# Kernel optimization log

Hardware: AMD Instinct MI355X
Metric: run time of the kernel (lower is better)

## Reference

```python
import jax, jax.numpy as jnp
import numpy as np

N_NODES = 50000
N_EDGES = 800000
F_IN, F_MID, F_OUT = 256, 128, 40


def gcn_conv(x, W, b, src, dst, n_nodes):
    # GCNConv (PyG defaults): add self-loops, symmetric normalization,
    # linear transform, scatter-sum to targets, then bias.
    h = x @ W  # [N, F_out]
    loop = jnp.arange(n_nodes, dtype=src.dtype)
    s = jnp.concatenate([src, loop])  # sources incl. self-loops
    d = jnp.concatenate([dst, loop])  # targets incl. self-loops
    deg = jax.ops.segment_sum(jnp.ones_like(d, dtype=h.dtype), d, num_segments=n_nodes)
    dinv = jnp.where(deg > 0, jax.lax.rsqrt(deg), 0.0)
    norm = dinv[s] * dinv[d]  # [E+N]
    msgs = h[s] * norm[:, None]  # [E+N, F_out]
    out = jax.ops.segment_sum(msgs, d, num_segments=n_nodes)
    return out + b


def setup_inputs() -> dict:
    key = jax.random.key(0)
    ks = jax.random.split(key, 8)
    x = jax.random.normal(ks[0], (N_NODES, F_IN), dtype=jnp.float32)
    edge_index = jax.random.randint(ks[1], (2, N_EDGES), 0, N_NODES, dtype=jnp.int64)

    def glorot(k, fin, fout):
        lim = float(np.sqrt(6.0 / (fin + fout)))
        return jax.random.uniform(k, (fin, fout), jnp.float32, -lim, lim)

    return {
        "x": x,
        "edge_index": edge_index,
        "W_in": glorot(ks[2], F_IN, F_MID),
        "b_in": jnp.zeros((F_MID,), jnp.float32),
        "W_mid": glorot(ks[3], F_MID, F_MID),
        "b_mid": jnp.zeros((F_MID,), jnp.float32),
        "W_out": glorot(ks[4], F_MID, F_OUT),
        "b_out": jnp.zeros((F_OUT,), jnp.float32),
    }


def reference(x, edge_index, W_in, b_in, W_mid, b_mid, W_out, b_out):
    src, dst = edge_index[0], edge_index[1]
    n = x.shape[0]
    # conv_in -> relu (dropout is identity in eval mode)
    h = jax.nn.relu(gcn_conv(x, W_in, b_in, src, dst, n))
    # middle GCN layer -> relu
    h = jax.nn.relu(gcn_conv(h, W_mid, b_mid, src, dst, n))
    # conv_out -> log_softmax over classes
    h = gcn_conv(h, W_out, b_out, src, dst, n)
    return jax.nn.log_softmax(h, axis=-1)
```

## Files before the change

kernel.cpp:

```cpp
#include <hip/hip_runtime.h>
#include <hip/hip_bf16.h>
#include <math.h>


#define F_IN  256
#define F_MID 128
#define F_OUT 40
#define PSH   9
#define BCAP2 10240

typedef __attribute__((ext_vector_type(8))) short bf16x8;
typedef __attribute__((ext_vector_type(4))) float f32x4;

union FragU {
    bf16x8 v;
    __hip_bfloat162 h2[4];
    uint4 u;
    unsigned short s[8];
};

__device__ __forceinline__ unsigned int f2bf(float f) {
    unsigned int u = __float_as_uint(f);
    return (u + 0x7fffu + ((u >> 16) & 1u)) >> 16;
}
__device__ __forceinline__ float bf_lo(unsigned int u) { return __uint_as_float(u << 16); }
__device__ __forceinline__ float bf_hi(unsigned int u) { return __uint_as_float(u & 0xffff0000u); }

__global__ __launch_bounds__(256) void k_prep0(int* __restrict__ bcur,
                                               const float* __restrict__ W1,
                                               const float* __restrict__ W2,
                                               const float* __restrict__ W3,
                                               unsigned short* __restrict__ Wp1,
                                               unsigned short* __restrict__ Wp2,
                                               unsigned short* __restrict__ Wp3) {
    if (blockIdx.x == 0) {
        if (threadIdx.x < 128) bcur[threadIdx.x] = 0;
        return;
    }
    int t = (blockIdx.x - 1) * 256 + threadIdx.x;
    const float* W; unsigned short* Wp; int M, Mp, kc, nn;
    if (t < 4096)      { W = W1; Wp = Wp1; M = 128; Mp = 128; kc = t >> 7; nn = t & 127; }
    else if (t < 6144) { t -= 4096; W = W2; Wp = Wp2; M = 128; Mp = 128; kc = t >> 7; nn = t & 127; }
    else if (t < 6912) { t -= 6144; W = W3; Wp = Wp3; M = 40;  Mp = 48;  kc = t / 48; nn = t % 48; }
    else return;
    FragU o;
#pragma unroll
    for (int j = 0; j < 8; ++j) {
        int k = kc * 8 + j;
        o.s[j] = (nn < M) ? (unsigned short)f2bf(W[k * M + nn]) : 0;
    }
    *(uint4*)&Wp[((size_t)kc * Mp + nn) * 8] = o.u;
}

__global__ __launch_bounds__(256) void k_bucket_gemm1(const int* __restrict__ src,
                                                      const int* __restrict__ dst,
                                                      unsigned int* __restrict__ bkt,
                                                      int* __restrict__ bcur,
                                                      int E, int nbBkt,
                                                      const float* __restrict__ x,
                                                      const unsigned short* __restrict__ Wp1,
                                                      unsigned short* __restrict__ hn, int n) {
    if (blockIdx.x < (unsigned)nbBkt) {
        __shared__ int hist[128], base[128], cur[128];
        const int t = threadIdx.x;
        if (t < 128) { hist[t] = 0; cur[t] = 0; }
        __syncthreads();
        const int e0 = blockIdx.x * 8192;
        unsigned int mye[32];
#pragma unroll
        for (int j = 0; j < 32; ++j) {
            int e = e0 + j * 256 + t;
            if (e < E) {
                mye[j] = ((unsigned int)dst[e] << 16) | (unsigned int)src[e];
                atomicAdd(&hist[mye[j] >> (16 + PSH)], 1);
            } else mye[j] = 0xffffffffu;
        }
        __syncthreads();
        if (t < 128) base[t] = hist[t] ? atomicAdd(&bcur[t], hist[t]) : 0;
        __syncthreads();
#pragma unroll
        for (int j = 0; j < 32; ++j) {
            if (mye[j] != 0xffffffffu) {
                int p = mye[j] >> (16 + PSH);
                int pos = base[p] + atomicAdd(&cur[p], 1);
                if (pos < BCAP2) bkt[(size_t)p * BCAP2 + pos] = mye[j];
            }
        }
        return;
    }
    const int t = threadIdx.x;
    const int w = t >> 6, lane = t & 63, sub = lane & 15, q = lane >> 4;
    const int row0 = (blockIdx.x - nbBkt) * 64 + w * 16;
    const int row = row0 + sub;
    const bool rv = row < n;
    const float* ap = x + (size_t)row * 256;

    float4 xv[16];
    if (rv) {
#pragma unroll
        for (int j = 0; j < 16; ++j)
            xv[j] = *(const float4*)(ap + (j >> 1) * 32 + q * 8 + (j & 1) * 4);
    } else {
#pragma unroll
        for (int j = 0; j < 16; ++j) xv[j] = make_float4(0.f, 0.f, 0.f, 0.f);
    }

    f32x4 acc[8];
#pragma unroll
    for (int cg = 0; cg < 8; ++cg) acc[cg] = (f32x4)0.f;

#pragma unroll
    for (int kk = 0; kk < 8; ++kk) {
        FragU af;
        float4 f0 = xv[2 * kk];
        float4 f1 = xv[2 * kk + 1];
        af.h2[0] = __float22bfloat162_rn(make_float2(f0.x, f0.y));
        af.h2[1] = __float22bfloat162_rn(make_float2(f0.z, f0.w));
        af.h2[2] = __float22bfloat162_rn(make_float2(f1.x, f1.y));
        af.h2[3] = __float22bfloat162_rn(make_float2(f1.z, f1.w));
        const unsigned short* wrow = Wp1 + (size_t)((kk * 4 + q) * 128 + sub) * 8;
#pragma unroll
        for (int cg = 0; cg < 8; ++cg) {
            bf16x8 b = *(const bf16x8*)(wrow + cg * 16 * 8);
            acc[cg] = __builtin_amdgcn_mfma_f32_16x16x32_bf16(b, af.v, acc[cg], 0, 0, 0);
        }
    }
    if (rv) {
#pragma unroll
        for (int cg = 0; cg < 8; ++cg) {
            uint2 pk;
            pk.x = f2bf(acc[cg][0]) | (f2bf(acc[cg][1]) << 16);
            pk.y = f2bf(acc[cg][2]) | (f2bf(acc[cg][3]) << 16);
            *(uint2*)(hn + (size_t)row * 128 + cg * 16 + q * 4) = pk;
        }
    }
}

__global__ __launch_bounds__(256) void k_sort(const unsigned int* __restrict__ bkt,
                                              const int* __restrict__ bcur,
                                              int* __restrict__ rofs,
                                              float* __restrict__ dinv,
                                              unsigned short* __restrict__ csr,
                                              int npart, int n) {
    __shared__ int hist[512];
    __shared__ int stmp[256];
    const int p = blockIdx.x;
    const int t = threadIdx.x;
    const int d0 = p << PSH;
    const int nd = min(512, n - d0);

    int bv = (t < p) ? bcur[t] : 0;
    bv = bv > BCAP2 ? BCAP2 : bv;
    stmp[t] = bv;
    hist[t] = 0; hist[t + 256] = 0;
    __syncthreads();
#pragma unroll
    for (int off = 128; off; off >>= 1) {
        if (t < off) stmp[t] += stmp[t + off];
        __syncthreads();
    }
    const int base = stmp[0];
    int np = bcur[p]; np = np > BCAP2 ? BCAP2 : np;
    const unsigned int* b = bkt + (size_t)p * BCAP2;

    for (int i0 = t; i0 < np; i0 += 2048) {
        unsigned int ee[8];
#pragma unroll
        for (int j = 0; j < 8; ++j) {
            int idx = i0 + j * 256;
            ee[j] = (idx < np) ? b[idx] : 0xffffffffu;
        }
#pragma unroll
        for (int j = 0; j < 8; ++j)
            if (ee[j] != 0xffffffffu)
                atomicAdd(&hist[(int)(ee[j] >> 16) - d0], 1);
    }
    __syncthreads();

    const int h0 = hist[2 * t], h1 = hist[2 * t + 1];
    __syncthreads();
    stmp[t] = h0 + h1;
    __syncthreads();
#pragma unroll
    for (int off = 1; off < 256; off <<= 1) {
        int xx = (t >= off) ? stmp[t - off] : 0;
        __syncthreads();
        stmp[t] += xx;
        __syncthreads();
    }
    const int excl = stmp[t] - (h0 + h1);

    hist[2 * t] = excl;
    hist[2 * t + 1] = excl + h0;
    if (2 * t < nd) {
        rofs[d0 + 2 * t] = base + excl;
        dinv[d0 + 2 * t] = rsqrtf((float)(h0 + 1));
    }
    if (2 * t + 1 < nd) {
        rofs[d0 + 2 * t + 1] = base + excl + h0;
        dinv[d0 + 2 * t + 1] = rsqrtf((float)(h1 + 1));
    }
    if (p == npart - 1 && t == 0) rofs[n] = base + np;
    __syncthreads();

    for (int i0 = t; i0 < np; i0 += 2048) {
        unsigned int ee[8];
#pragma unroll
        for (int j = 0; j < 8; ++j) {
            int idx = i0 + j * 256;
            ee[j] = (idx < np) ? b[idx] : 0xffffffffu;
        }
#pragma unroll
        for (int j = 0; j < 8; ++j) {
            if (ee[j] != 0xffffffffu) {
                int ld = (int)(ee[j] >> 16) - d0;
                int pos = atomicAdd(&hist[ld], 1);
                csr[base + pos] = (unsigned short)(ee[j] & 0xffffu);
            }
        }
    }
}

template <int K>
__global__ __launch_bounds__(256) void gemm_mfma_bf16A(const unsigned short* __restrict__ A,
                                                       const unsigned short* __restrict__ Wp,
                                                       unsigned short* __restrict__ hn, int n) {
    const int t = threadIdx.x;
    const int w = t >> 6, lane = t & 63, sub = lane & 15, q = lane >> 4;
    const int row0 = blockIdx.x * 64 + w * 16;
    const int row = row0 + sub;
    const bool rv = row < n;
    const unsigned short* ap = A + (size_t)row * K;

    uint4 xv[K / 32];
    if (rv) {
#pragma unroll
        for (int j = 0; j < K / 32; ++j)
            xv[j] = *(const uint4*)(ap + j * 32 + q * 8);
    } else {
#pragma unroll
        for (int j = 0; j < K / 32; ++j) xv[j] = make_uint4(0, 0, 0, 0);
    }

    f32x4 acc[8];
#pragma unroll
    for (int cg = 0; cg < 8; ++cg) acc[cg] = (f32x4)0.f;

#pragma unroll
    for (int kk = 0; kk < K / 32; ++kk) {
        FragU af; af.u = xv[kk];
        const unsigned short* wrow = Wp + (size_t)((kk * 4 + q) * 128 + sub) * 8;
#pragma unroll
        for (int cg = 0; cg < 8; ++cg) {
            bf16x8 b = *(const bf16x8*)(wrow + cg * 16 * 8);
            acc[cg] = __builtin_amdgcn_mfma_f32_16x16x32_bf16(b, af.v, acc[cg], 0, 0, 0);
        }
    }

    if (rv) {
#pragma unroll
        for (int cg = 0; cg < 8; ++cg) {
            uint2 pk;
            pk.x = f2bf(acc[cg][0]) | (f2bf(acc[cg][1]) << 16);
            pk.y = f2bf(acc[cg][2]) | (f2bf(acc[cg][3]) << 16);
            *(uint2*)(hn + (size_t)row * 128 + cg * 16 + q * 4) = pk;
        }
    }
}

__global__ __launch_bounds__(256) void gemm_mfma_m40(const unsigned short* __restrict__ A,
                                                     const unsigned short* __restrict__ Wp,
                                                     unsigned short* __restrict__ hn, int n) {
    const int K = 128;
    const int t = threadIdx.x;
    const int w = t >> 6, lane = t & 63, sub = lane & 15, q = lane >> 4;
    const int row0 = blockIdx.x * 64 + w * 16;
    const int row = row0 + sub;
    const bool rv = row < n;
    const unsigned short* ap = A + (size_t)row * K;

    uint4 xv[4];
    if (rv) {
#pragma unroll
        for (int j = 0; j < 4; ++j)
            xv[j] = *(const uint4*)(ap + j * 32 + q * 8);
    } else {
#pragma unroll
        for (int j = 0; j < 4; ++j) xv[j] = make_uint4(0, 0, 0, 0);
    }

    f32x4 acc[3];
#pragma unroll
    for (int cg = 0; cg < 3; ++cg) acc[cg] = (f32x4)0.f;

#pragma unroll
    for (int kk = 0; kk < 4; ++kk) {
        FragU af; af.u = xv[kk];
        const unsigned short* wrow = Wp + (size_t)((kk * 4 + q) * 48 + sub) * 8;
#pragma unroll
        for (int cg = 0; cg < 3; ++cg) {
            bf16x8 b = *(const bf16x8*)(wrow + cg * 16 * 8);
            acc[cg] = __builtin_amdgcn_mfma_f32_16x16x32_bf16(b, af.v, acc[cg], 0, 0, 0);
        }
    }

    if (rv) {
#pragma unroll
        for (int cg = 0; cg < 3; ++cg) {
            int feat = cg * 16 + q * 4;
            if (feat < 40) {
                uint2 pk;
                pk.x = f2bf(acc[cg][0]) | (f2bf(acc[cg][1]) << 16);
                pk.y = f2bf(acc[cg][2]) | (f2bf(acc[cg][3]) << 16);
                *(uint2*)(hn + (size_t)row * 40 + feat) = pk;
            }
        }
    }
}

__device__ __forceinline__ void acc_row(float* acc, uint4 u, float dv) {
    acc[0] += dv * bf_lo(u.x); acc[1] += dv * bf_hi(u.x);
    acc[2] += dv * bf_lo(u.y); acc[3] += dv * bf_hi(u.y);
    acc[4] += dv * bf_lo(u.z); acc[5] += dv * bf_hi(u.z);
    acc[6] += dv * bf_lo(u.w); acc[7] += dv * bf_hi(u.w);
}

__global__ __launch_bounds__(256) void agg128_bf16(const unsigned short* __restrict__ hn,
                                                   const int* __restrict__ rofs,
                                                   const unsigned short* __restrict__ csr,
                                                   const float* __restrict__ dinv,
                                                   const float* __restrict__ bias,
                                                   unsigned short* __restrict__ obf, int n) {
    int wid = (blockIdx.x * 256 + threadIdx.x) >> 6;
    if (wid >= n) return;
    const int v = wid;
    const int lane = threadIdx.x & 63;
    const int q = lane >> 4;
    const int sub = lane & 15;
    float acc[8];
#pragma unroll
    for (int k = 0; k < 8; ++k) acc[k] = 0.f;
    const int e0 = rofs[v];
    const int total = rofs[v + 1] - e0 + 1;

    for (int i0 = 0; i0 < total; i0 += 32) {
        int sA[8]; float dA[8];
#pragma unroll
        for (int j = 0; j < 8; ++j) {
            int ix = i0 + q + 4 * j;
            bool ok = ix < total;
            int s = ok ? ((ix == 0) ? v : (int)csr[e0 + ix - 1]) : v;
            sA[j] = s;
            dA[j] = ok ? dinv[s] : 0.f;
        }
#pragma unroll
        for (int j = 0; j < 8; ++j) {
            uint4 u = *(const uint4*)(hn + (size_t)sA[j] * 128 + sub * 8);
            acc_row(acc, u, dA[j]);
        }
    }
#pragma unroll
    for (int k = 0; k < 8; ++k) {
        acc[k] += __shfl_xor(acc[k], 16);
        acc[k] += __shfl_xor(acc[k], 32);
    }
    if (q == 0) {
        float dv = dinv[v];
        float4 b0 = *(const float4*)(bias + sub * 8);
        float4 b1 = *(const float4*)(bias + sub * 8 + 4);
        float o[8];
        o[0] = fmaxf(dv * acc[0] + b0.x, 0.f);
        o[1] = fmaxf(dv * acc[1] + b0.y, 0.f);
        o[2] = fmaxf(dv * acc[2] + b0.z, 0.f);
        o[3] = fmaxf(dv * acc[3] + b0.w, 0.f);
        o[4] = fmaxf(dv * acc[4] + b1.x, 0.f);
        o[5] = fmaxf(dv * acc[5] + b1.y, 0.f);
        o[6] = fmaxf(dv * acc[6] + b1.z, 0.f);
        o[7] = fmaxf(dv * acc[7] + b1.w, 0.f);
        uint4 pk;
        pk.x = f2bf(o[0]) | (f2bf(o[1]) << 16);
        pk.y = f2bf(o[2]) | (f2bf(o[3]) << 16);
        pk.z = f2bf(o[4]) | (f2bf(o[5]) << 16);
        pk.w = f2bf(o[6]) | (f2bf(o[7]) << 16);
        *(uint4*)(obf + (size_t)v * 128 + sub * 8) = pk;
    }
}

__global__ __launch_bounds__(256) void agg40_lsm_bf16(const unsigned short* __restrict__ hn,
                                                      const int* __restrict__ rofs,
                                                      const unsigned short* __restrict__ csr,
                                                      const float* __restrict__ dinv,
                                                      const float* __restrict__ bias,
                                                      float* __restrict__ out, int n) {
    int wid = (blockIdx.x * 256 + threadIdx.x) >> 6;
    if (wid >= n) return;
    const int v = wid;
    const int lane = threadIdx.x & 63;
    const int h = lane >> 5;
    const int sl = lane & 31;
    const bool act = sl < 20;
    float a0 = 0.f, a1 = 0.f;
    const int e0 = rofs[v];
    const int total = rofs[v + 1] - e0 + 1;

    for (int i0 = 0; i0 < total; i0 += 16) {
        int sA[8];
        unsigned char okA[8];
#pragma unroll
        for (int j = 0; j < 8; ++j) {
            int ix = i0 + h + 2 * j;
            bool ok = ix < total;
            sA[j] = ok ? ((ix == 0) ? v : (int)csr[e0 + ix - 1]) : v;
            okA[j] = ok ? 1 : 0;
        }
        if (act) {
#pragma unroll
            for (int j = 0; j < 8; ++j) {
                float d = okA[j] ? dinv[sA[j]] : 0.f;
                unsigned int u = *(const unsigned int*)(hn + (size_t)sA[j] * 40 + sl * 2);
                a0 += d * bf_lo(u);
                a1 += d * bf_hi(u);
            }
        }
    }
    a0 += __shfl_xor(a0, 32);
    a1 += __shfl_xor(a1, 32);
    float dv = dinv[v];
    float v0 = act ? (dv * a0 + bias[sl * 2])     : -3.402823466e38f;
    float v1 = act ? (dv * a1 + bias[sl * 2 + 1]) : -3.402823466e38f;
    float m = fmaxf(v0, v1);
#pragma unroll
    for (int off = 16; off; off >>= 1) m = fmaxf(m, __shfl_xor(m, off));
    float p = act ? (__expf(v0 - m) + __expf(v1 - m)) : 0.f;
#pragma unroll
    for (int off = 16; off; off >>= 1) p += __shfl_xor(p, off);
    if (h == 0 && act) {
        float ls = __logf(p);
        *(float2*)(out + (size_t)v * 40 + sl * 2) = make_float2(v0 - m - ls, v1 - m - ls);
    }
}


extern "C" void kernel_launch(void* const* d_in, const int* in_sizes, int n_in,
                              void* d_out, int out_size, void* d_ws, size_t ws_size,
                              hipStream_t stream) {
    const float* x     = (const float*)d_in[0];
    const int*   ei    = (const int*)d_in[1];
    const float* W_in  = (const float*)d_in[2];
    const float* b_in  = (const float*)d_in[3];
    const float* W_mid = (const float*)d_in[4];
    const float* b_mid = (const float*)d_in[5];
    const float* W_out = (const float*)d_in[6];
    const float* b_out = (const float*)d_in[7];
    float* out = (float*)d_out;

    const int N = in_sizes[0] / F_IN;
    const int E = in_sizes[1] / 2;
    const int* srcp = ei;
    const int* dstp = ei + E;
    const int npart = (N + (1 << PSH) - 1) >> PSH;

    char* w = (char*)d_ws;
    unsigned short* hn  = (unsigned short*)w; w += (size_t)N * 128 * 2;
    unsigned short* obf = (unsigned short*)w; w += (size_t)N * 128 * 2;
    float* dinv = (float*)w; w += (size_t)N * 4;
    int* bcur   = (int*)w;   w += 512;
    int* rofs   = (int*)w;   w += (size_t)(N + 1) * 4 + 12;
    unsigned int* bkt = (unsigned int*)w; w += (size_t)npart * BCAP2 * 4;
    unsigned short* csr = (unsigned short*)w; w += (size_t)E * 2 + 128;
    unsigned short* Wp1 = (unsigned short*)((((size_t)w) + 15) & ~(size_t)15); w = (char*)Wp1 + 32 * 128 * 8 * 2;
    unsigned short* Wp2 = (unsigned short*)w; w += 16 * 128 * 8 * 2;
    unsigned short* Wp3 = (unsigned short*)w; w += 16 * 48 * 8 * 2;

    const int nbW = (N * 64 + 255) / 256;
    const int nbG = (N + 63) / 64;
    const int nbBkt = (E + 8191) / 8192;

    k_prep0<<<28, 256, 0, stream>>>(bcur, W_in, W_mid, W_out, Wp1, Wp2, Wp3);
    k_bucket_gemm1<<<nbBkt + nbG, 256, 0, stream>>>(srcp, dstp, bkt, bcur, E, nbBkt,
                                                    x, Wp1, hn, N);
    k_sort<<<npart, 256, 0, stream>>>(bkt, bcur, rofs, dinv, csr, npart, N);

    agg128_bf16<<<nbW, 256, 0, stream>>>(hn, rofs, csr, dinv, b_in, obf, N);
    gemm_mfma_bf16A<128><<<nbG, 256, 0, stream>>>(obf, Wp2, hn, N);
    agg128_bf16<<<nbW, 256, 0, stream>>>(hn, rofs, csr, dinv, b_mid, obf, N);
    gemm_mfma_m40<<<nbG, 256, 0, stream>>>(obf, Wp3, hn, N);
    agg40_lsm_bf16<<<nbW, 256, 0, stream>>>(hn, rofs, csr, dinv, b_out, out, N);
}
```

Measured before the change: 262.1 us.

## Fuse aggregation with next-layer GEMM and pre-scale features by source dinv

Restructures the pipeline so that each 128-wide aggregation runs in the same kernel as the following layer's MFMA GEMM, staging the aggregated rows in LDS. This removes the intermediate obf round-trip and two kernel launches. Source-side normalization is folded into the stored features: a new scale pass multiplies layer-1 outputs by dinv, and the GEMM epilogues multiply by dinv, so the gathers no longer load dinv per edge. A zero padding row at index n lets out-of-range lanes read harmless data. Weight prep is merged into the bucket kernel, and GEMM1 is co-scheduled with the sort kernel. The costs are an extra full pass over hn1, one node per 16 lanes in the fused kernel, and an extra bf16 rounding from the pre-scaling.

```diff
diff --git a/kernel.cpp b/kernel.cpp
--- a/kernel.cpp
+++ b/kernel.cpp
@@ -26,71 +26,160 @@
 __device__ __forceinline__ float bf_lo(unsigned int u) { return __uint_as_float(u << 16); }
 __device__ __forceinline__ float bf_hi(unsigned int u) { return __uint_as_float(u & 0xffff0000u); }
 
-__global__ __launch_bounds__(256) void k_prep0(int* __restrict__ bcur,
-                                               const float* __restrict__ W1,
-                                               const float* __restrict__ W2,
-                                               const float* __restrict__ W3,
-                                               unsigned short* __restrict__ Wp1,
-                                               unsigned short* __restrict__ Wp2,
-                                               unsigned short* __restrict__ Wp3) {
-    if (blockIdx.x == 0) {
-        if (threadIdx.x < 128) bcur[threadIdx.x] = 0;
+__device__ __forceinline__ void add_row(float* acc, uint4 u) {
+    acc[0] += bf_lo(u.x); acc[1] += bf_hi(u.x);
+    acc[2] += bf_lo(u.y); acc[3] += bf_hi(u.y);
+    acc[4] += bf_lo(u.z); acc[5] += bf_hi(u.z);
+    acc[6] += bf_lo(u.w); acc[7] += bf_hi(u.w);
+}
+
+__global__ __launch_bounds__(256) void k_bucket_prep(const int* __restrict__ src,
+                                                     const int* __restrict__ dst,
+                                                     unsigned int* __restrict__ bkt,
+                                                     int* __restrict__ bcur,
+                                                     int E, int nbBkt,
+                                                     const float* __restrict__ W1,
+                                                     const float* __restrict__ W2,
+                                                     const float* __restrict__ W3,
+                                                     unsigned short* __restrict__ Wp1,
+                                                     unsigned short* __restrict__ Wp2,
+                                                     unsigned short* __restrict__ Wp3) {
+    if (blockIdx.x >= (unsigned)nbBkt) {
+        int t = (blockIdx.x - nbBkt) * 256 + threadIdx.x;
+        const float* W; unsigned short* Wp; int M, Mp, kc, nn;
+        if (t < 4096)      { W = W1; Wp = Wp1; M = 128; Mp = 128; kc = t >> 7; nn = t & 127; }
+        else if (t < 6144) { t -= 4096; W = W2; Wp = Wp2; M = 128; Mp = 128; kc = t >> 7; nn = t & 127; }
+        else if (t < 6912) { t -= 6144; W = W3; Wp = Wp3; M = 40;  Mp = 48;  kc = t / 48; nn = t % 48; }
+        else return;
+        FragU o;
+#pragma unroll
+        for (int j = 0; j < 8; ++j) {
+            int k = kc * 8 + j;
+            o.s[j] = (nn < M) ? (unsigned short)f2bf(W[k * M + nn]) : 0;
+        }
+        *(uint4*)&Wp[((size_t)kc * Mp + nn) * 8] = o.u;
         return;
     }
-    int t = (blockIdx.x - 1) * 256 + threadIdx.x;
-    const float* W; unsigned short* Wp; int M, Mp, kc, nn;
-    if (t < 4096)      { W = W1; Wp = Wp1; M = 128; Mp = 128; kc = t >> 7; nn = t & 127; }
-    else if (t < 6144) { t -= 4096; W = W2; Wp = Wp2; M = 128; Mp = 128; kc = t >> 7; nn = t & 127; }
-    else if (t < 6912) { t -= 6144; W = W3; Wp = Wp3; M = 40;  Mp = 48;  kc = t / 48; nn = t % 48; }
-    else return;
-    FragU o;
-#pragma unroll
-    for (int j = 0; j < 8; ++j) {
-        int k = kc * 8 + j;
-        o.s[j] = (nn < M) ? (unsigned short)f2bf(W[k * M + nn]) : 0;
-    }
-    *(uint4*)&Wp[((size_t)kc * Mp + nn) * 8] = o.u;
-}
-
-__global__ __launch_bounds__(256) void k_bucket_gemm1(const int* __restrict__ src,
-                                                      const int* __restrict__ dst,
-                                                      unsigned int* __restrict__ bkt,
-                                                      int* __restrict__ bcur,
-                                                      int E, int nbBkt,
-                                                      const float* __restrict__ x,
-                                                      const unsigned short* __restrict__ Wp1,
-                                                      unsigned short* __restrict__ hn, int n) {
-    if (blockIdx.x < (unsigned)nbBkt) {
-        __shared__ int hist[128], base[128], cur[128];
+    __shared__ int hist[128], base[128], cur[128];
+    const int t = threadIdx.x;
+    if (t < 128) { hist[t] = 0; cur[t] = 0; }
+    __syncthreads();
+    const int e0 = blockIdx.x * 8192;
+    unsigned int mye[32];
+#pragma unroll
+    for (int j = 0; j < 32; ++j) {
+        int e = e0 + j * 256 + t;
+        if (e < E) {
+            mye[j] = ((unsigned int)dst[e] << 16) | (unsigned int)src[e];
+            atomicAdd(&hist[mye[j] >> (16 + PSH)], 1);
+        } else mye[j] = 0xffffffffu;
+    }
+    __syncthreads();
+    if (t < 128) base[t] = hist[t] ? atomicAdd(&bcur[t], hist[t]) : 0;
+    __syncthreads();
+#pragma unroll
+    for (int j = 0; j < 32; ++j) {
+        if (mye[j] != 0xffffffffu) {
+            int p = mye[j] >> (16 + PSH);
+            int pos = base[p] + atomicAdd(&cur[p], 1);
+            if (pos < BCAP2) bkt[(size_t)p * BCAP2 + pos] = mye[j];
+        }
+    }
+}
+
+__global__ __launch_bounds__(256) void k_gemm1_sort(const unsigned int* __restrict__ bkt,
+                                                    const int* __restrict__ bcur,
+                                                    int* __restrict__ rofs,
+                                                    float* __restrict__ dinv,
+                                                    unsigned short* __restrict__ csr,
+                                                    int nbG, int npart,
+                                                    const float* __restrict__ x,
+                                                    const unsigned short* __restrict__ Wp1,
+                                                    unsigned short* __restrict__ hn, int n) {
+    __shared__ int sh[768];
+    if (blockIdx.x >= (unsigned)nbG) {
+        int* hist = sh;
+        int* stmp = sh + 512;
+        const int p = blockIdx.x - nbG;
         const int t = threadIdx.x;
-        if (t < 128) { hist[t] = 0; cur[t] = 0; }
+        const int d0 = p << PSH;
+        const int nd = min(512, n - d0);
+
+        int bv = (t < p) ? bcur[t] : 0;
+        bv = bv > BCAP2 ? BCAP2 : bv;
+        stmp[t] = bv;
+        hist[t] = 0; hist[t + 256] = 0;
         __syncthreads();
-        const int e0 = blockIdx.x * 8192;
-        unsigned int mye[32];
-#pragma unroll
-        for (int j = 0; j < 32; ++j) {
-            int e = e0 + j * 256 + t;
-            if (e < E) {
-                mye[j] = ((unsigned int)dst[e] << 16) | (unsigned int)src[e];
-                atomicAdd(&hist[mye[j] >> (16 + PSH)], 1);
-            } else mye[j] = 0xffffffffu;
+#pragma unroll
+        for (int off = 128; off; off >>= 1) {
+            if (t < off) stmp[t] += stmp[t + off];
+            __syncthreads();
+        }
+        const int base = stmp[0];
+        int np = bcur[p]; np = np > BCAP2 ? BCAP2 : np;
+        const unsigned int* b = bkt + (size_t)p * BCAP2;
+
+        for (int i0 = t; i0 < np; i0 += 2048) {
+            unsigned int ee[8];
+#pragma unroll
+            for (int j = 0; j < 8; ++j) {
+                int idx = i0 + j * 256;
+                ee[j] = (idx < np) ? b[idx] : 0xffffffffu;
+            }
+#pragma unroll
+            for (int j = 0; j < 8; ++j)
+                if (ee[j] != 0xffffffffu)
+                    atomicAdd(&hist[(int)(ee[j] >> 16) - d0], 1);
         }
         __syncthreads();
-        if (t < 128) base[t] = hist[t] ? atomicAdd(&bcur[t], hist[t]) : 0;
+
+        const int h0 = hist[2 * t], h1 = hist[2 * t + 1];
         __syncthreads();
-#pragma unroll
-        for (int j = 0; j < 32; ++j) {
-            if (mye[j] != 0xffffffffu) {
-                int p = mye[j] >> (16 + PSH);
-                int pos = base[p] + atomicAdd(&cur[p], 1);
-                if (pos < BCAP2) bkt[(size_t)p * BCAP2 + pos] = mye[j];
+        stmp[t] = h0 + h1;
+        __syncthreads();
+#pragma unroll
+        for (int off = 1; off < 256; off <<= 1) {
+            int xx = (t >= off) ? stmp[t - off] : 0;
+            __syncthreads();
+            stmp[t] += xx;
+            __syncthreads();
+        }
+        const int excl = stmp[t] - (h0 + h1);
+
+        hist[2 * t] = excl;
+        hist[2 * t + 1] = excl + h0;
+        if (2 * t < nd) {
+            rofs[d0 + 2 * t] = base + excl;
+            dinv[d0 + 2 * t] = rsqrtf((float)(h0 + 1));
+        }
+        if (2 * t + 1 < nd) {
+            rofs[d0 + 2 * t + 1] = base + excl + h0;
+            dinv[d0 + 2 * t + 1] = rsqrtf((float)(h1 + 1));
+        }
+        if (p == npart - 1 && t == 0) rofs[n] = base + np;
+        __syncthreads();
+
+        for (int i0 = t; i0 < np; i0 += 2048) {
+            unsigned int ee[8];
+#pragma unroll
+            for (int j = 0; j < 8; ++j) {
+                int idx = i0 + j * 256;
+                ee[j] = (idx < np) ? b[idx] : 0xffffffffu;
+            }
+#pragma unroll
+            for (int j = 0; j < 8; ++j) {
+                if (ee[j] != 0xffffffffu) {
+                    int ld = (int)(ee[j] >> 16) - d0;
+                    int pos = atomicAdd(&hist[ld], 1);
+                    csr[base + pos] = (unsigned short)(ee[j] & 0xffffu);
+                }
             }
         }
         return;
     }
     const int t = threadIdx.x;
     const int w = t >> 6, lane = t & 63, sub = lane & 15, q = lane >> 4;
-    const int row0 = (blockIdx.x - nbBkt) * 64 + w * 16;
+    const int row0 = blockIdx.x * 64 + w * 16;
     const int row = row0 + sub;
     const bool rv = row < n;
     const float* ap = x + (size_t)row * 256;
@@ -136,257 +225,143 @@
     }
 }
 
-__global__ __launch_bounds__(256) void k_sort(const unsigned int* __restrict__ bkt,
-                                              const int* __restrict__ bcur,
-                                              int* __restrict__ rofs,
-                                              float* __restrict__ dinv,
-                                              unsigned short* __restrict__ csr,
-                                              int npart, int n) {
-    __shared__ int hist[512];
-    __shared__ int stmp[256];
-    const int p = blockIdx.x;
-    const int t = threadIdx.x;
-    const int d0 = p << PSH;
-    const int nd = min(512, n - d0);
-
-    int bv = (t < p) ? bcur[t] : 0;
-    bv = bv > BCAP2 ? BCAP2 : bv;
-    stmp[t] = bv;
-    hist[t] = 0; hist[t + 256] = 0;
-    __syncthreads();
-#pragma unroll
-    for (int off = 128; off; off >>= 1) {
-        if (t < off) stmp[t] += stmp[t + off];
-        __syncthreads();
-    }
-    const int base = stmp[0];
-    int np = bcur[p]; np = np > BCAP2 ? BCAP2 : np;
-    const unsigned int* b = bkt + (size_t)p * BCAP2;
-
-    for (int i0 = t; i0 < np; i0 += 2048) {
-        unsigned int ee[8];
-#pragma unroll
-        for (int j = 0; j < 8; ++j) {
-            int idx = i0 + j * 256;
-            ee[j] = (idx < np) ? b[idx] : 0xffffffffu;
-        }
-#pragma unroll
-        for (int j = 0; j < 8; ++j)
-            if (ee[j] != 0xffffffffu)
-                atomicAdd(&hist[(int)(ee[j] >> 16) - d0], 1);
-    }
-    __syncthreads();
-
-    const int h0 = hist[2 * t], h1 = hist[2 * t + 1];
-    __syncthreads();
-    stmp[t] = h0 + h1;
-    __syncthreads();
-#pragma unroll
-    for (int off = 1; off < 256; off <<= 1) {
-        int xx = (t >= off) ? stmp[t - off] : 0;
-        __syncthreads();
-        stmp[t] += xx;
-        __syncthreads();
-    }
-    const int excl = stmp[t] - (h0 + h1);
-
-    hist[2 * t] = excl;
-    hist[2 * t + 1] = excl + h0;
-    if (2 * t < nd) {
-        rofs[d0 + 2 * t] = base + excl;
-        dinv[d0 + 2 * t] = rsqrtf((float)(h0 + 1));
-    }
-    if (2 * t + 1 < nd) {
-        rofs[d0 + 2 * t + 1] = base + excl + h0;
-        dinv[d0 + 2 * t + 1] = rsqrtf((float)(h1 + 1));
-    }
-    if (p == npart - 1 && t == 0) rofs[n] = base + np;
-    __syncthreads();
-
-    for (int i0 = t; i0 < np; i0 += 2048) {
-        unsigned int ee[8];
-#pragma unroll
-        for (int j = 0; j < 8; ++j) {
-            int idx = i0 + j * 256;
-            ee[j] = (idx < np) ? b[idx] : 0xffffffffu;
-        }
-#pragma unroll
-        for (int j = 0; j < 8; ++j) {
-            if (ee[j] != 0xffffffffu) {
-                int ld = (int)(ee[j] >> 16) - d0;
-                int pos = atomicAdd(&hist[ld], 1);
-                csr[base + pos] = (unsigned short)(ee[j] & 0xffffu);
-            }
-        }
-    }
-}
-
-template <int K>
-__global__ __launch_bounds__(256) void gemm_mfma_bf16A(const unsigned short* __restrict__ A,
-                                                       const unsigned short* __restrict__ Wp,
-                                                       unsigned short* __restrict__ hn, int n) {
+__global__ __launch_bounds__(256) void k_scale(unsigned short* __restrict__ hn1,
+                                               const float* __restrict__ dinv,
+                                               unsigned short* __restrict__ hn2,
+                                               unsigned short* __restrict__ hn3,
+                                               int n) {
+    const int nt = n * 16;
+    for (int i = blockIdx.x * 256 + threadIdx.x; i < nt; i += gridDim.x * 256) {
+        int row = i >> 4;
+        float dv = dinv[row];
+        uint4 u = *(const uint4*)(hn1 + (size_t)i * 8);
+        uint4 o;
+        o.x = f2bf(dv * bf_lo(u.x)) | (f2bf(dv * bf_hi(u.x)) << 16);
+        o.y = f2bf(dv * bf_lo(u.y)) | (f2bf(dv * bf_hi(u.y)) << 16);
+        o.z = f2bf(dv * bf_lo(u.z)) | (f2bf(dv * bf_hi(u.z)) << 16);
+        o.w = f2bf(dv * bf_lo(u.w)) | (f2bf(dv * bf_hi(u.w)) << 16);
+        *(uint4*)(hn1 + (size_t)i * 8) = o;
+    }
+    if (blockIdx.x == 0) {
+        int t = threadIdx.x;
+        uint4 z = make_uint4(0, 0, 0, 0);
+        if (t < 16) *(uint4*)(hn1 + (size_t)n * 128 + t * 8) = z;
+        else if (t < 32) *(uint4*)(hn2 + (size_t)n * 128 + (t - 16) * 8) = z;
+        else if (t < 52) ((unsigned int*)(hn3 + (size_t)n * 40))[t - 32] = 0;
+    }
+}
+
+template <int MOUT, int MP>
+__global__ __launch_bounds__(256) void k_agg_gemm(const unsigned short* __restrict__ hnS,
+                                                  const int* __restrict__ rofs,
+                                                  const unsigned short* __restrict__ csr,
+                                                  const float* __restrict__ dinv,
+                                                  const float* __restrict__ bias,
+                                                  const unsigned short* __restrict__ Wp,
+                                                  unsigned short* __restrict__ hout,
+                                                  int n) {
+    __shared__ unsigned short arows[16][136];
     const int t = threadIdx.x;
     const int w = t >> 6, lane = t & 63, sub = lane & 15, q = lane >> 4;
-    const int row0 = blockIdx.x * 64 + w * 16;
-    const int row = row0 + sub;
-    const bool rv = row < n;
-    const unsigned short* ap = A + (size_t)row * K;
-
-    uint4 xv[K / 32];
-    if (rv) {
-#pragma unroll
-        for (int j = 0; j < K / 32; ++j)
-            xv[j] = *(const uint4*)(ap + j * 32 + q * 8);
-    } else {
-#pragma unroll
-        for (int j = 0; j < K / 32; ++j) xv[j] = make_uint4(0, 0, 0, 0);
-    }
-
-    f32x4 acc[8];
-#pragma unroll
-    for (int cg = 0; cg < 8; ++cg) acc[cg] = (f32x4)0.f;
-
-#pragma unroll
-    for (int kk = 0; kk < K / 32; ++kk) {
-        FragU af; af.u = xv[kk];
-        const unsigned short* wrow = Wp + (size_t)((kk * 4 + q) * 128 + sub) * 8;
-#pragma unroll
-        for (int cg = 0; cg < 8; ++cg) {
-            bf16x8 b = *(const bf16x8*)(wrow + cg * 16 * 8);
-            acc[cg] = __builtin_amdgcn_mfma_f32_16x16x32_bf16(b, af.v, acc[cg], 0, 0, 0);
-        }
-    }
-
-    if (rv) {
-#pragma unroll
-        for (int cg = 0; cg < 8; ++cg) {
-            uint2 pk;
-            pk.x = f2bf(acc[cg][0]) | (f2bf(acc[cg][1]) << 16);
-            pk.y = f2bf(acc[cg][2]) | (f2bf(acc[cg][3]) << 16);
-            *(uint2*)(hn + (size_t)row * 128 + cg * 16 + q * 4) = pk;
-        }
-    }
-}
-
-__global__ __launch_bounds__(256) void gemm_mfma_m40(const unsigned short* __restrict__ A,
-                                                     const unsigned short* __restrict__ Wp,
-                                                     unsigned short* __restrict__ hn, int n) {
-    const int K = 128;
-    const int t = threadIdx.x;
-    const int w = t >> 6, lane = t & 63, sub = lane & 15, q = lane >> 4;
-    const int row0 = blockIdx.x * 64 + w * 16;
-    const int row = row0 + sub;
-    const bool rv = row < n;
-    const unsigned short* ap = A + (size_t)row * K;
-
-    uint4 xv[4];
-    if (rv) {
-#pragma unroll
-        for (int j = 0; j < 4; ++j)
-            xv[j] = *(const uint4*)(ap + j * 32 + q * 8);
-    } else {
-#pragma unroll
-        for (int j = 0; j < 4; ++j) xv[j] = make_uint4(0, 0, 0, 0);
-    }
-
-    f32x4 acc[3];
-#pragma unroll
-    for (int cg = 0; cg < 3; ++cg) acc[cg] = (f32x4)0.f;
-
-#pragma unroll
-    for (int kk = 0; kk < 4; ++kk) {
-        FragU af; af.u = xv[kk];
-        const unsigned short* wrow = Wp + (size_t)((kk * 4 + q) * 48 + sub) * 8;
-#pragma unroll
-        for (int cg = 0; cg < 3; ++cg) {
-            bf16x8 b = *(const bf16x8*)(wrow + cg * 16 * 8);
-            acc[cg] = __builtin_amdgcn_mfma_f32_16x16x32_bf16(b, af.v, acc[cg], 0, 0, 0);
-        }
-    }
-
-    if (rv) {
-#pragma unroll
-        for (int cg = 0; cg < 3; ++cg) {
-            int feat = cg * 16 + q * 4;
-            if (feat < 40) {
-                uint2 pk;
-                pk.x = f2bf(acc[cg][0]) | (f2bf(acc[cg][1]) << 16);
-                pk.y = f2bf(acc[cg][2]) | (f2bf(acc[cg][3]) << 16);
-                *(uint2*)(hn + (size_t)row * 40 + feat) = pk;
-            }
-        }
-    }
-}
-
-__device__ __forceinline__ void acc_row(float* acc, uint4 u, float dv) {
-    acc[0] += dv * bf_lo(u.x); acc[1] += dv * bf_hi(u.x);
-    acc[2] += dv * bf_lo(u.y); acc[3] += dv * bf_hi(u.y);
-    acc[4] += dv * bf_lo(u.z); acc[5] += dv * bf_hi(u.z);
-    acc[6] += dv * bf_lo(u.w); acc[7] += dv * bf_hi(u.w);
-}
-
-__global__ __launch_bounds__(256) void agg128_bf16(const unsigned short* __restrict__ hn,
-                                                   const int* __restrict__ rofs,
-                                                   const unsigned short* __restrict__ csr,
-                                                   const float* __restrict__ dinv,
-                                                   const float* __restrict__ bias,
-                                                   unsigned short* __restrict__ obf, int n) {
-    int wid = (blockIdx.x * 256 + threadIdx.x) >> 6;
-    if (wid >= n) return;
-    const int v = wid;
-    const int lane = threadIdx.x & 63;
-    const int q = lane >> 4;
-    const int sub = lane & 15;
+    const int v0 = blockIdx.x * 16;
+    const int r = w * 4 + q;
+    const int node = v0 + r;
+    const bool nv = node < n;
+
     float acc[8];
 #pragma unroll
     for (int k = 0; k < 8; ++k) acc[k] = 0.f;
-    const int e0 = rofs[v];
-    const int total = rofs[v + 1] - e0 + 1;
-
-    for (int i0 = 0; i0 < total; i0 += 32) {
-        int sA[8]; float dA[8];
-#pragma unroll
-        for (int j = 0; j < 8; ++j) {
-            int ix = i0 + q + 4 * j;
-            bool ok = ix < total;
-            int s = ok ? ((ix == 0) ? v : (int)csr[e0 + ix - 1]) : v;
-            sA[j] = s;
-            dA[j] = ok ? dinv[s] : 0.f;
-        }
-#pragma unroll
-        for (int j = 0; j < 8; ++j) {
-            uint4 u = *(const uint4*)(hn + (size_t)sA[j] * 128 + sub * 8);
-            acc_row(acc, u, dA[j]);
-        }
-    }
-#pragma unroll
-    for (int k = 0; k < 8; ++k) {
-        acc[k] += __shfl_xor(acc[k], 16);
-        acc[k] += __shfl_xor(acc[k], 32);
-    }
-    if (q == 0) {
-        float dv = dinv[v];
+
+    int e0 = 0, deg = 0;
+    if (nv) { e0 = rofs[node]; deg = rofs[node + 1] - e0; }
+    const int total = nv ? deg + 1 : 0;
+    int ea = (sub < deg) ? (int)csr[e0 + sub] : n;
+    int eb = (16 + sub < deg) ? (int)csr[e0 + 16 + sub] : n;
+    const int lim = (total < 33) ? total : 33;
+
+    for (int ix0 = 0; ix0 < lim; ix0 += 8) {
+        int sA[8];
+#pragma unroll
+        for (int jj = 0; jj < 8; ++jj) {
+            int ix = ix0 + jj;
+            int em = (ix - 1) & 15;
+            int srcA = __shfl(ea, (lane & 48) + em);
+            int srcB = __shfl(eb, (lane & 48) + em);
+            int s = (ix - 1 < 16) ? srcA : srcB;
+            s = (ix == 0) ? node : s;
+            sA[jj] = (ix < lim) ? s : n;
+        }
+        uint4 u[8];
+#pragma unroll
+        for (int jj = 0; jj < 8; ++jj)
+            u[jj] = *(const uint4*)(hnS + (size_t)sA[jj] * 128 + sub * 8);
+#pragma unroll
+        for (int jj = 0; jj < 8; ++jj) add_row(acc, u[jj]);
+    }
+    for (int ix = 33; ix < total; ++ix) {
+        int s = (int)csr[e0 + ix - 1];
+        uint4 u = *(const uint4*)(hnS + (size_t)s * 128 + sub * 8);
+        add_row(acc, u);
+    }
+
+    uint4 pk = make_uint4(0, 0, 0, 0);
+    if (nv) {
+        float dv = dinv[node];
         float4 b0 = *(const float4*)(bias + sub * 8);
         float4 b1 = *(const float4*)(bias + sub * 8 + 4);
-        float o[8];
-        o[0] = fmaxf(dv * acc[0] + b0.x, 0.f);
-        o[1] = fmaxf(dv * acc[1] + b0.y, 0.f);
-        o[2] = fmaxf(dv * acc[2] + b0.z, 0.f);
-        o[3] = fmaxf(dv * acc[3] + b0.w, 0.f);
-        o[4] = fmaxf(dv * acc[4] + b1.x, 0.f);
-        o[5] = fmaxf(dv * acc[5] + b1.y, 0.f);
-        o[6] = fmaxf(dv * acc[6] + b1.z, 0.f);
-        o[7] = fmaxf(dv * acc[7] + b1.w, 0.f);
-        uint4 pk;
-        pk.x = f2bf(o[0]) | (f2bf(o[1]) << 16);
-        pk.y = f2bf(o[2]) | (f2bf(o[3]) << 16);
-        pk.z = f2bf(o[4]) | (f2bf(o[5]) << 16);
-        pk.w = f2bf(o[6]) | (f2bf(o[7]) << 16);
-        *(uint4*)(obf + (size_t)v * 128 + sub * 8) = pk;
-    }
-}
-
-__global__ __launch_bounds__(256) void agg40_lsm_bf16(const unsigned short* __restrict__ hn,
+        float o0 = fmaxf(dv * acc[0] + b0.x, 0.f);
+        float o1 = fmaxf(dv * acc[1] + b0.y, 0.f);
+        float o2 = fmaxf(dv * acc[2] + b0.z, 0.f);
+        float o3 = fmaxf(dv * acc[3] + b0.w, 0.f);
+        float o4 = fmaxf(dv * acc[4] + b1.x, 0.f);
+        float o5 = fmaxf(dv * acc[5] + b1.y, 0.f);
+        float o6 = fmaxf(dv * acc[6] + b1.z, 0.f);
+        float o7 = fmaxf(dv * acc[7] + b1.w, 0.f);
+        pk.x = f2bf(o0) | (f2bf(o1) << 16);
+        pk.y = f2bf(o2) | (f2bf(o3) << 16);
+        pk.z = f2bf(o4) | (f2bf(o5) << 16);
+        pk.w = f2bf(o6) | (f2bf(o7) << 16);
+    }
+    *(uint4*)&arows[r][sub * 8] = pk;
+    __syncthreads();
+
+    const int NCG = MP / 16;
+    const int NCGW = (MP == 128) ? 2 : 1;
+    f32x4 gacc[2];
+#pragma unroll
+    for (int i = 0; i < 2; ++i) gacc[i] = (f32x4)0.f;
+
+#pragma unroll
+    for (int kstep = 0; kstep < 4; ++kstep) {
+        FragU af;
+        af.u = *(const uint4*)&arows[sub][kstep * 32 + q * 8];
+#pragma unroll
+        for (int i = 0; i < NCGW; ++i) {
+            int cg = w * NCGW + i;
+            if (cg < NCG) {
+                bf16x8 b = *(const bf16x8*)(Wp + (size_t)((kstep * 4 + q) * MP + cg * 16 + sub) * 8);
+                gacc[i] = __builtin_amdgcn_mfma_f32_16x16x32_bf16(b, af.v, gacc[i], 0, 0, 0);
+            }
+        }
+    }
+    const int orow = v0 + sub;
+    if (orow < n) {
+        float dvr = dinv[orow];
+#pragma unroll
+        for (int i = 0; i < NCGW; ++i) {
+            int cg = w * NCGW + i;
+            int feat = cg * 16 + q * 4;
+            if (cg < NCG && feat < MOUT) {
+                uint2 p2;
+                p2.x = f2bf(dvr * gacc[i][0]) | (f2bf(dvr * gacc[i][1]) << 16);
+                p2.y = f2bf(dvr * gacc[i][2]) | (f2bf(dvr * gacc[i][3]) << 16);
+                *(uint2*)(hout + (size_t)orow * MOUT + feat) = p2;
+            }
+        }
+    }
+}
+
+__global__ __launch_bounds__(256) void agg40_lsm_bf16(const unsigned short* __restrict__ hnS,
                                                       const int* __restrict__ rofs,
                                                       const unsigned short* __restrict__ csr,
                                                       const float* __restrict__ dinv,
@@ -405,21 +380,18 @@
 
     for (int i0 = 0; i0 < total; i0 += 16) {
         int sA[8];
-        unsigned char okA[8];
 #pragma unroll
         for (int j = 0; j < 8; ++j) {
             int ix = i0 + h + 2 * j;
-            bool ok = ix < total;
-            sA[j] = ok ? ((ix == 0) ? v : (int)csr[e0 + ix - 1]) : v;
-            okA[j] = ok ? 1 : 0;
+            int s = (ix < total) ? ((ix == 0) ? v : (int)csr[e0 + ix - 1]) : n;
+            sA[j] = s;
         }
         if (act) {
 #pragma unroll
             for (int j = 0; j < 8; ++j) {
-                float d = okA[j] ? dinv[sA[j]] : 0.f;
-                unsigned int u = *(const unsigned int*)(hn + (size_t)sA[j] * 40 + sl * 2);
-                a0 += d * bf_lo(u);
-                a1 += d * bf_hi(u);
+                unsigned int u = *(const unsigned int*)(hnS + (size_t)sA[j] * 40 + sl * 2);
+                a0 += bf_lo(u);
+                a1 += bf_hi(u);
             }
         }
     }
@@ -461,8 +433,9 @@
     const int npart = (N + (1 << PSH) - 1) >> PSH;
 
     char* w = (char*)d_ws;
-    unsigned short* hn  = (unsigned short*)w; w += (size_t)N * 128 * 2;
-    unsigned short* obf = (unsigned short*)w; w += (size_t)N * 128 * 2;
+    unsigned short* hn1 = (unsigned short*)w; w += (size_t)(N + 1) * 128 * 2;
+    unsigned short* hn2 = (unsigned short*)w; w += (size_t)(N + 1) * 128 * 2;
+    unsigned short* hn3 = (unsigned short*)w; w += (size_t)(N + 1) * 40 * 2 + 16;
     float* dinv = (float*)w; w += (size_t)N * 4;
     int* bcur   = (int*)w;   w += 512;
     int* rofs   = (int*)w;   w += (size_t)(N + 1) * 4 + 12;
@@ -474,16 +447,16 @@
 
     const int nbW = (N * 64 + 255) / 256;
     const int nbG = (N + 63) / 64;
+    const int nbF = (N + 15) / 16;
     const int nbBkt = (E + 8191) / 8192;
 
-    k_prep0<<<28, 256, 0, stream>>>(bcur, W_in, W_mid, W_out, Wp1, Wp2, Wp3);
-    k_bucket_gemm1<<<nbBkt + nbG, 256, 0, stream>>>(srcp, dstp, bkt, bcur, E, nbBkt,
-                                                    x, Wp1, hn, N);
-    k_sort<<<npart, 256, 0, stream>>>(bkt, bcur, rofs, dinv, csr, npart, N);
-
-    agg128_bf16<<<nbW, 256, 0, stream>>>(hn, rofs, csr, dinv, b_in, obf, N);
-    gemm_mfma_bf16A<128><<<nbG, 256, 0, stream>>>(obf, Wp2, hn, N);
-    agg128_bf16<<<nbW, 256, 0, stream>>>(hn, rofs, csr, dinv, b_mid, obf, N);
-    gemm_mfma_m40<<<nbG, 256, 0, stream>>>(obf, Wp3, hn, N);
-    agg40_lsm_bf16<<<nbW, 256, 0, stream>>>(hn, rofs, csr, dinv, b_out, out, N);
-}
+    hipMemsetAsync(bcur, 0, 512, stream);
+    k_bucket_prep<<<nbBkt + 27, 256, 0, stream>>>(srcp, dstp, bkt, bcur, E, nbBkt,
+                                                  W_in, W_mid, W_out, Wp1, Wp2, Wp3);
+    k_gemm1_sort<<<nbG + npart, 256, 0, stream>>>(bkt, bcur, rofs, dinv, csr,
+                                                  nbG, npart, x, Wp1, hn1, N);
+    k_scale<<<2048, 256, 0, stream>>>(hn1, dinv, hn2, hn3, N);
+    k_agg_gemm<128, 128><<<nbF, 256, 0, stream>>>(hn1, rofs, csr, dinv, b_in, Wp2, hn2, N);
+    k_agg_gemm<40, 48><<<nbF, 256, 0, stream>>>(hn2, rofs, csr, dinv, b_mid, Wp3, hn3, N);
+    agg40_lsm_bf16<<<nbW, 256, 0, stream>>>(hn3, rofs, csr, dinv, b_out, out, N);
+}
```

Result: faster. 229.8 us (-12.3%).
